# Kernel optimization log

Hardware: AMD Instinct MI355X
Metric: run time of the kernel (lower is better)

## Reference

```python
import jax, jax.numpy as jnp
import numpy as np

N_FILE, N_CLASS, N_FUNC = 50_000, 150_000, 300_000
E = 300_000
D = 128
L = 2  # num_layers

# (src_type, dst_type, conv_idx, edge_arg_name); conv_idx: 0=file,1=file_call,2=own,3=call
RELATIONS = [
    ("FILE", "CLASS", 0, "e_f_own_c"),
    ("FILE", "FUNCTION", 0, "e_f_own_fn"),
    ("FILE", "FUNCTION", 1, "e_f_call_fn"),
    ("FILE", "FILE", 1, "e_f_imp_f"),
    ("FILE", "CLASS", 1, "e_f_imp_c"),
    ("FILE", "FUNCTION", 1, "e_f_imp_fn"),
    ("CLASS", "CLASS", 2, "e_c_own_c"),
    ("CLASS", "FUNCTION", 2, "e_c_own_fn"),
    ("FUNCTION", "CLASS", 2, "e_fn_own_c"),
    ("FUNCTION", "FUNCTION", 2, "e_fn_own_fn"),
    ("CLASS", "FUNCTION", 3, "e_c_call_fn"),
    ("CLASS", "CLASS", 3, "e_c_inh_c"),
    ("FUNCTION", "FUNCTION", 3, "e_fn_call_fn"),
]
N_OF = {"FILE": N_FILE, "CLASS": N_CLASS, "FUNCTION": N_FUNC}


def _edges(key, n_src, n_dst):
    k1, k2 = jax.random.split(key)
    src = jax.random.randint(k1, (E,), 0, n_src, dtype=jnp.int32)
    dst = jax.random.randint(k2, (E,), 0, n_dst, dtype=jnp.int32)
    return jnp.stack([src, dst])  # [2, E]


def setup_inputs() -> dict:
    key = jax.random.key(0)
    ks = jax.random.split(key, 20)
    inp = {
        "x_file": jax.random.normal(ks[0], (N_FILE, D), jnp.float32),
        "x_class": jax.random.normal(ks[1], (N_CLASS, D), jnp.float32),
        "x_func": jax.random.normal(ks[2], (N_FUNC, D), jnp.float32),
        "Wl": jax.random.normal(ks[3], (L, 4, D, D), jnp.float32) * 0.05,
        "bl": jax.random.normal(ks[4], (L, 4, D), jnp.float32) * 0.05,
        "Wr": jax.random.normal(ks[5], (L, 4, D, D), jnp.float32) * 0.05,
    }
    for i, (s, t, _ci, name) in enumerate(RELATIONS):
        inp[name] = _edges(ks[6 + i], N_OF[s], N_OF[t])
    return inp


def _sage(x_src, x_dst, edges, Wl_, bl_, Wr_):
    """SAGEConv with mean aggregation: lin_l(scatter_mean(x_src[src] -> dst)) + lin_r(x_dst)."""
    src, dst = edges[0], edges[1]
    n_dst = x_dst.shape[0]
    msg = x_src[src]  # [E, D] gather
    agg = jax.ops.segment_sum(msg, dst, num_segments=n_dst)  # [n_dst, D]
    cnt = jax.ops.segment_sum(jnp.ones((msg.shape[0],), msg.dtype), dst, num_segments=n_dst)
    mean = agg / jnp.maximum(cnt, 1.0)[:, None]  # degree-0 nodes -> 0
    return mean @ Wl_ + bl_ + x_dst @ Wr_


def _forward(x_file, x_class, x_func, Wl, bl, Wr, edge_dict):
    h = {"FILE": x_file, "CLASS": x_class, "FUNCTION": x_func}
    for layer in range(L):
        outs = {"FILE": [], "CLASS": [], "FUNCTION": []}
        for s, t, ci, name in RELATIONS:
            outs[t].append(
                _sage(h[s], h[t], edge_dict[name], Wl[layer, ci], bl[layer, ci], Wr[layer, ci])
            )
        # HeteroConv aggr='mean' across relations per dst type, then ReLU
        h = {t: jax.nn.relu(sum(v) / float(len(v))) for t, v in outs.items()}
    # original returns a dict; concatenate in fixed order FILE, CLASS, FUNCTION
    return jnp.concatenate([h["FILE"], h["CLASS"], h["FUNCTION"]], axis=0)


def reference(x_file, x_class, x_func, Wl, bl, Wr,
              e_f_own_c, e_f_own_fn, e_f_call_fn, e_f_imp_f, e_f_imp_c, e_f_imp_fn,
              e_c_own_c, e_c_own_fn, e_fn_own_c, e_fn_own_fn,
              e_c_call_fn, e_c_inh_c, e_fn_call_fn):
    edge_dict = {
        "e_f_own_c": e_f_own_c, "e_f_own_fn": e_f_own_fn, "e_f_call_fn": e_f_call_fn,
        "e_f_imp_f": e_f_imp_f, "e_f_imp_c": e_f_imp_c, "e_f_imp_fn": e_f_imp_fn,
        "e_c_own_c": e_c_own_c, "e_c_own_fn": e_c_own_fn, "e_fn_own_c": e_fn_own_c,
        "e_fn_own_fn": e_fn_own_fn, "e_c_call_fn": e_c_call_fn, "e_c_inh_c": e_c_inh_c,
        "e_fn_call_fn": e_fn_call_fn,
    }
    return _forward(x_file, x_class, x_func, Wl, bl, Wr, edge_dict)
```

## Files before the change

### kernel.cpp

```cpp
#include <hip/hip_runtime.h>
#include <hip/hip_bf16.h>
#include <stdint.h>

typedef unsigned short u16;
typedef unsigned int u32;

#define NFILE 50000
#define NCLASS 150000
#define NFUNC 300000
#define NTOT 500000
#define EDG 300000
#define NRELS 13
#define RTOT 2900000

typedef __attribute__((ext_vector_type(8))) short bf16x8;
typedef __attribute__((ext_vector_type(4))) float f32x4;

__device__ __forceinline__ u16 f2b(float v){
    u32 u = __float_as_uint(v);
    u += 0x7fffu + ((u >> 16) & 1u);
    return (u16)(u >> 16);
}
__device__ __forceinline__ float b2f(u16 b){
    return __uint_as_float(((u32)b) << 16);
}
__device__ __forceinline__ u32 pack2(float a, float b){
    return (u32)f2b(a) | ((u32)f2b(b) << 16);
}

struct EdgePtrs { const int* e[NRELS]; };
struct RelMeta  { int base[NRELS]; };

__global__ void prep_weights(const float* __restrict__ Wl, const float* __restrict__ bl,
                             const float* __restrict__ Wr,
                             u16* __restrict__ WlT, u16* __restrict__ WrSumT,
                             float* __restrict__ blSum){
    int tid = blockIdx.x * 256 + threadIdx.x;
    if (tid >= 2 * 16384) return;
    int l   = tid >> 14;
    int rem = tid & 16383;
    int n   = rem >> 7;
    int k   = rem & 127;
    const int m[3][4] = {{0,1,0,0},{1,1,2,1},{1,2,2,2}};
    #pragma unroll
    for (int ci = 0; ci < 4; ++ci){
        float w = Wl[(((l*4)+ci)*128 + k)*128 + n];
        WlT[((l*4+ci)*128 + n)*128 + k] = f2b(w);
    }
    #pragma unroll
    for (int t = 0; t < 3; ++t){
        float s = 0.f;
        #pragma unroll
        for (int ci = 0; ci < 4; ++ci)
            s += (float)m[t][ci] * Wr[(((l*4)+ci)*128 + k)*128 + n];
        WrSumT[((l*3+t)*128 + n)*128 + k] = f2b(s);
    }
    if (k == 0){
        #pragma unroll
        for (int t = 0; t < 3; ++t){
            float s = 0.f;
            #pragma unroll
            for (int ci = 0; ci < 4; ++ci)
                s += (float)m[t][ci] * bl[(l*4+ci)*128 + n];
            blSum[(l*3+t)*128 + n] = s;
        }
    }
}

__global__ void count_kernel(EdgePtrs ep, RelMeta rm, int* __restrict__ off){
    int rel = blockIdx.y;
    int e = blockIdx.x * 256 + threadIdx.x;
    if (e >= EDG) return;
    int dst = ep.e[rel][EDG + e];
    atomicAdd(&off[rm.base[rel] + dst], 1);
}

__global__ void scan1(int* __restrict__ data, int* __restrict__ bsums, int n){
    __shared__ int sd[256];
    int tid = threadIdx.x;
    long base = (long)blockIdx.x * 2048 + (long)tid * 8;
    int v[8]; int tot = 0;
    #pragma unroll
    for (int i = 0; i < 8; ++i){
        long ix = base + i;
        v[i] = (ix < n) ? data[ix] : 0;
        tot += v[i];
    }
    sd[tid] = tot;
    __syncthreads();
    for (int s = 1; s < 256; s <<= 1){
        int t = (tid >= s) ? sd[tid - s] : 0;
        __syncthreads();
        sd[tid] += t;
        __syncthreads();
    }
    int incl = sd[tid];
    int excl = incl - tot;
    if (tid == 255 && bsums) bsums[blockIdx.x] = incl;
    int run = excl;
    #pragma unroll
    for (int i = 0; i < 8; ++i){
        long ix = base + i;
        if (ix < n) data[ix] = run;
        run += v[i];
    }
}

__global__ void scan_add(int* __restrict__ data, const int* __restrict__ bsums, int n){
    long i = (long)blockIdx.x * 256 + threadIdx.x;
    if (i < n) data[i] += bsums[i >> 11];
}

__global__ void fill_kernel(EdgePtrs ep, RelMeta rm, int* __restrict__ off, int* __restrict__ csr){
    int rel = blockIdx.y;
    int e = blockIdx.x * 256 + threadIdx.x;
    if (e >= EDG) return;
    int src = ep.e[rel][e];
    int dst = ep.e[rel][EDG + e];
    int pos = atomicAdd(&off[rm.base[rel] + dst], 1);
    csr[pos] = src;
}

struct FusedArgs {
    const void* sp0[4];
    const void* sp1[4];
    int b0[4], b1[4], nR[4];
    const u16* wl[4];
    int nG;
    const u16* wself;
    const float* bias;
};

template<bool SRC32, bool FINAL>
__global__ __launch_bounds__(256) void fused_kernel(
    const int* __restrict__ off, const int* __restrict__ csr,
    FusedArgs fa, const void* __restrict__ xdst,
    void* __restrict__ outp, int nRows, float invR)
{
    __shared__ u16 wlds[16384];
    __shared__ u16 meanB[8192];
    int tid = threadIdx.x, wave = tid >> 6, lane = tid & 63;
    int row0 = blockIdx.x * 64;
    int rlo = lane & 15, blk = lane >> 4;

    f32x4 acc[8];
    #pragma unroll
    for (int nt = 0; nt < 8; ++nt) acc[nt] = (f32x4){0.f, 0.f, 0.f, 0.f};

    for (int g = 0; g < fa.nG; ++g){
        __syncthreads();
        {
            const u16* WT = fa.wl[g];
            #pragma unroll
            for (int c = 0; c < 8; ++c){
                int i = c * 2048 + tid * 8;
                int n = i >> 7;
                int boff = (i * 2) ^ ((n & 7) << 4);
                *(uint4*)((char*)wlds + boff) = *(const uint4*)((const char*)WT + (long)i * 2);
            }
        }
        for (int rr = 0; rr < 4; ++rr){
            int row = wave * 16 + rr * 4 + blk;
            long grow = (long)row0 + row;
            bool valid = grow < nRows;
            float a[8];
            #pragma unroll
            for (int k = 0; k < 8; ++k) a[k] = 0.f;
            for (int r = 0; r < fa.nR[g]; ++r){
                const void* sp = r ? fa.sp1[g] : fa.sp0[g];
                long gr = (long)(r ? fa.b1[g] : fa.b0[g]) + grow;
                int st = 0, en = 0;
                if (valid){ st = (gr > 0) ? off[gr - 1] : 0; en = off[gr]; }
                float s[8], s2[8];
                #pragma unroll
                for (int k = 0; k < 8; ++k){ s[k] = 0.f; s2[k] = 0.f; }
                int j = st;
                for (; j + 1 < en; j += 2){
                    long i0 = csr[j], i1 = csr[j + 1];
                    if (SRC32){
                        const float* p0 = (const float*)sp + i0 * 128 + rlo * 8;
                        const float* p1 = (const float*)sp + i1 * 128 + rlo * 8;
                        float4 u0 = *(const float4*)p0, u1 = *(const float4*)(p0 + 4);
                        float4 v0 = *(const float4*)p1, v1 = *(const float4*)(p1 + 4);
                        s[0] += u0.x; s[1] += u0.y; s[2] += u0.z; s[3] += u0.w;
                        s[4] += u1.x; s[5] += u1.y; s[6] += u1.z; s[7] += u1.w;
                        s2[0] += v0.x; s2[1] += v0.y; s2[2] += v0.z; s2[3] += v0.w;
                        s2[4] += v1.x; s2[5] += v1.y; s2[6] += v1.z; s2[7] += v1.w;
                    } else {
                        uint4 u = *(const uint4*)((const u16*)sp + i0 * 128 + rlo * 8);
                        uint4 v = *(const uint4*)((const u16*)sp + i1 * 128 + rlo * 8);
                        s[0] += b2f((u16)(u.x & 0xffff)); s[1] += b2f((u16)(u.x >> 16));
                        s[2] += b2f((u16)(u.y & 0xffff)); s[3] += b2f((u16)(u.y >> 16));
                        s[4] += b2f((u16)(u.z & 0xffff)); s[5] += b2f((u16)(u.z >> 16));
                        s[6] += b2f((u16)(u.w & 0xffff)); s[7] += b2f((u16)(u.w >> 16));
                        s2[0] += b2f((u16)(v.x & 0xffff)); s2[1] += b2f((u16)(v.x >> 16));
                        s2[2] += b2f((u16)(v.y & 0xffff)); s2[3] += b2f((u16)(v.y >> 16));
                        s2[4] += b2f((u16)(v.z & 0xffff)); s2[5] += b2f((u16)(v.z >> 16));
                        s2[6] += b2f((u16)(v.w & 0xffff)); s2[7] += b2f((u16)(v.w >> 16));
                    }
                }
                if (j < en){
                    long i0 = csr[j];
                    if (SRC32){
                        const float* p0 = (const float*)sp + i0 * 128 + rlo * 8;
                        float4 u0 = *(const float4*)p0, u1 = *(const float4*)(p0 + 4);
                        s[0] += u0.x; s[1] += u0.y; s[2] += u0.z; s[3] += u0.w;
                        s[4] += u1.x; s[5] += u1.y; s[6] += u1.z; s[7] += u1.w;
                    } else {
                        uint4 u = *(const uint4*)((const u16*)sp + i0 * 128 + rlo * 8);
                        s[0] += b2f((u16)(u.x & 0xffff)); s[1] += b2f((u16)(u.x >> 16));
                        s[2] += b2f((u16)(u.y & 0xffff)); s[3] += b2f((u16)(u.y >> 16));
                        s[4] += b2f((u16)(u.z & 0xffff)); s[5] += b2f((u16)(u.z >> 16));
                        s[6] += b2f((u16)(u.w & 0xffff)); s[7] += b2f((u16)(u.w >> 16));
                    }
                }
                if (en > st){
                    float inv = 1.f / (float)(en - st);
                    #pragma unroll
                    for (int k = 0; k < 8; ++k) a[k] += (s[k] + s2[k]) * inv;
                }
            }
            uint4 w;
            w.x = pack2(a[0], a[1]); w.y = pack2(a[2], a[3]);
            w.z = pack2(a[4], a[5]); w.w = pack2(a[6], a[7]);
            int boff = (row * 256 + rlo * 16) ^ ((row & 7) << 4);
            *(uint4*)((char*)meanB + boff) = w;
        }
        __syncthreads();
        int arow = wave * 16 + rlo;
        #pragma unroll
        for (int s4 = 0; s4 < 4; ++s4){
            int aoff = (arow * 256 + s4 * 64 + blk * 16) ^ ((arow & 7) << 4);
            bf16x8 afr = *(const bf16x8*)((const char*)meanB + aoff);
            #pragma unroll
            for (int nt = 0; nt < 8; ++nt){
                int n = nt * 16 + rlo;
                int boff = (n * 256 + s4 * 64 + blk * 16) ^ ((n & 7) << 4);
                bf16x8 bfr = *(const bf16x8*)((const char*)wlds + boff);
                acc[nt] = __builtin_amdgcn_mfma_f32_16x16x32_bf16(afr, bfr, acc[nt], 0, 0, 0);
            }
        }
    }

    __syncthreads();
    {
        const u16* WT = fa.wself;
        #pragma unroll
        for (int c = 0; c < 8; ++c){
            int i = c * 2048 + tid * 8;
            int n = i >> 7;
            int boff = (i * 2) ^ ((n & 7) << 4);
            *(uint4*)((char*)wlds + boff) = *(const uint4*)((const char*)WT + (long)i * 2);
        }
    }
    __syncthreads();
    {
        long arow = (long)row0 + wave * 16 + rlo;
        if (arow >= nRows) arow = nRows - 1;
        bf16x8 af[4];
        if (SRC32){
            const float* A = (const float*)xdst + arow * 128;
            #pragma unroll
            for (int s4 = 0; s4 < 4; ++s4){
                float4 u0 = *(const float4*)(A + s4 * 32 + blk * 8);
                float4 u1 = *(const float4*)(A + s4 * 32 + blk * 8 + 4);
                bf16x8 t;
                t[0] = (short)f2b(u0.x); t[1] = (short)f2b(u0.y);
                t[2] = (short)f2b(u0.z); t[3] = (short)f2b(u0.w);
                t[4] = (short)f2b(u1.x); t[5] = (short)f2b(u1.y);
                t[6] = (short)f2b(u1.z); t[7] = (short)f2b(u1.w);
                af[s4] = t;
            }
        } else {
            const u16* A = (const u16*)xdst + arow * 128;
            #pragma unroll
            for (int s4 = 0; s4 < 4; ++s4)
                af[s4] = *(const bf16x8*)(A + s4 * 32 + blk * 8);
        }
        #pragma unroll
        for (int s4 = 0; s4 < 4; ++s4){
            #pragma unroll
            for (int nt = 0; nt < 8; ++nt){
                int n = nt * 16 + rlo;
                int boff = (n * 256 + s4 * 64 + blk * 16) ^ ((n & 7) << 4);
                bf16x8 bfr = *(const bf16x8*)((const char*)wlds + boff);
                acc[nt] = __builtin_amdgcn_mfma_f32_16x16x32_bf16(af[s4], bfr, acc[nt], 0, 0, 0);
            }
        }
    }

    long rb = (long)row0 + wave * 16 + blk * 4;
    #pragma unroll
    for (int nt = 0; nt < 8; ++nt){
        int cx = nt * 16 + rlo;
        float b = fa.bias[cx];
        #pragma unroll
        for (int j = 0; j < 4; ++j){
            long r = rb + j;
            if (r < nRows){
                float v = fmaxf(0.f, (acc[nt][j] + b) * invR);
                if (FINAL) ((float*)outp)[r * 128 + cx] = v;
                else       ((u16*)outp)[r * 128 + cx] = f2b(v);
            }
        }
    }
}

extern "C" void kernel_launch(void* const* d_in, const int* in_sizes, int n_in,
                              void* d_out, int out_size, void* d_ws, size_t ws_size,
                              hipStream_t stream){
    const float* xF  = (const float*)d_in[0];
    const float* xC  = (const float*)d_in[1];
    const float* xFn = (const float*)d_in[2];
    const float* Wl  = (const float*)d_in[3];
    const float* bl  = (const float*)d_in[4];
    const float* Wr  = (const float*)d_in[5];

    static const int relDstT[NRELS] = {1,2,2,0,1,2,1,2,1,2,2,1,2};
    static const int relSrcT[NRELS] = {0,0,0,0,0,0,1,1,2,2,1,1,2};
    const int nOf[3] = {NFILE, NCLASS, NFUNC};

    EdgePtrs ep;
    for (int r = 0; r < NRELS; ++r) ep.e[r] = (const int*)d_in[6 + r];
    RelMeta rm;
    {
        int a = 0;
        for (int r = 0; r < NRELS; ++r){ rm.base[r] = a; a += nOf[relDstT[r]]; }
    }

    char* ws = (char*)d_ws;
    size_t wo = 0;
    auto walloc = [&](size_t bytes) -> void* {
        void* p = ws + wo;
        wo = (wo + bytes + 255) & ~(size_t)255;
        return p;
    };
    int* off    = (int*)walloc((size_t)RTOT * 4);
    int* bsums  = (int*)walloc(8192);
    int* csr    = (int*)walloc((size_t)NRELS * EDG * 4);
    u16* h1     = (u16*)walloc((size_t)NTOT * 128 * 2);
    u16* WlT    = (u16*)walloc(2 * 4 * 16384 * 2);
    u16* WrSumT = (u16*)walloc(2 * 3 * 16384 * 2);
    float* blSum= (float*)walloc(2 * 3 * 128 * 4);

    prep_weights<<<128, 256, 0, stream>>>(Wl, bl, Wr, WlT, WrSumT, blSum);

    hipMemsetAsync(off, 0, (size_t)RTOT * 4, stream);
    dim3 egrid((EDG + 255) / 256, NRELS);
    count_kernel<<<egrid, 256, 0, stream>>>(ep, rm, off);
    int nb1 = (RTOT + 2047) / 2048;
    scan1<<<nb1, 256, 0, stream>>>(off, bsums, RTOT);
    scan1<<<1, 256, 0, stream>>>(bsums, (int*)nullptr, nb1);
    scan_add<<<(RTOT + 255) / 256, 256, 0, stream>>>(off, bsums, RTOT);
    fill_kernel<<<egrid, 256, 0, stream>>>(ep, rm, off, csr);

    float* outSeg[3] = {
        (float*)d_out,
        (float*)d_out + (long)NFILE * 128,
        (float*)d_out + (long)(NFILE + NCLASS) * 128
    };
    u16* hSeg[3] = {
        h1,
        h1 + (long)NFILE * 128,
        h1 + (long)(NFILE + NCLASS) * 128
    };
    const void* xSeg[3] = {xF, xC, xFn};
    const float invR[3] = {1.f, 0.2f, 1.f / 7.f};

    struct GDef { int ci, r0, r1; };
    static const GDef gF [1] = {{1, 3, -1}};
    static const GDef gC [4] = {{0, 0, -1}, {1, 4, -1}, {2, 6, 8}, {3, 11, -1}};
    static const GDef gFn[4] = {{0, 1, -1}, {1, 2, 5}, {2, 7, 9}, {3, 10, 12}};
    const GDef* gdefs[3] = {gF, gC, gFn};
    const int nGof[3] = {1, 4, 4};

    for (int layer = 0; layer < 2; ++layer){
        bool l0 = (layer == 0);
        for (int t = 0; t < 3; ++t){
            FusedArgs fa;
            fa.nG = nGof[t];
            for (int g = 0; g < fa.nG; ++g){
                const GDef gd = gdefs[t][g];
                fa.wl[g] = WlT + (layer * 4 + gd.ci) * 16384;
                fa.b0[g] = rm.base[gd.r0];
                fa.sp0[g] = l0 ? xSeg[relSrcT[gd.r0]] : (const void*)hSeg[relSrcT[gd.r0]];
                if (gd.r1 >= 0){
                    fa.nR[g] = 2;
                    fa.b1[g] = rm.base[gd.r1];
                    fa.sp1[g] = l0 ? xSeg[relSrcT[gd.r1]] : (const void*)hSeg[relSrcT[gd.r1]];
                } else {
                    fa.nR[g] = 1;
                    fa.b1[g] = 0;
                    fa.sp1[g] = nullptr;
                }
            }
            for (int g = fa.nG; g < 4; ++g){
                fa.wl[g] = nullptr; fa.b0[g] = fa.b1[g] = fa.nR[g] = 0;
                fa.sp0[g] = fa.sp1[g] = nullptr;
            }
            fa.wself = WrSumT + (layer * 3 + t) * 16384;
            fa.bias  = blSum + (layer * 3 + t) * 128;

            int n = nOf[t];
            int gb = (n + 63) / 64;
            const void* xdst = l0 ? xSeg[t] : (const void*)hSeg[t];
            void* outp = l0 ? (void*)hSeg[t] : (void*)outSeg[t];
            if (l0) fused_kernel<true , false><<<gb, 256, 0, stream>>>(off, csr, fa, xdst, outp, n, invR[t]);
            else    fused_kernel<false, true ><<<gb, 256, 0, stream>>>(off, csr, fa, xdst, outp, n, invR[t]);
        }
    }
}
```

Measured before the change: 2.909 ms.

## Specialize fused SAGE kernel per node type and pair relation groups per phase

Replaces the runtime-looped fused kernel with one specialized per destination type, whose slot-to-group mapping is fixed at compile time. Mean aggregation for two groups now runs per phase into double shared buffers, and the first two neighbour gathers are issued unconditionally with clamped indices and zero weights to hide latency. Weight tiles are no longer staged in LDS; MFMA B fragments are read directly from global memory (cached). This cuts LDS usage and barriers to target higher occupancy (launch bounds 4). The cost is redundant gathers for low-degree nodes and uncoalesced global weight reads.

```diff
diff --git a/kernel.cpp b/kernel.cpp
--- a/kernel.cpp
+++ b/kernel.cpp
@@ -12,6 +12,7 @@
 #define EDG 300000
 #define NRELS 13
 #define RTOT 2900000
+#define CSRMAX (NRELS * EDG)
 
 typedef __attribute__((ext_vector_type(8))) short bf16x8;
 typedef __attribute__((ext_vector_type(4))) float f32x4;
@@ -121,24 +122,93 @@
     csr[pos] = src;
 }
 
-struct FusedArgs {
-    const void* sp0[4];
-    const void* sp1[4];
-    int b0[4], b1[4], nR[4];
-    const u16* wl[4];
-    int nG;
+
+template<int T> struct Meta;
+template<> struct Meta<0>{ static constexpr int NG=1, NS=1;
+    static constexpr int sg[1]={0}; };
+template<> struct Meta<1>{ static constexpr int NG=4, NS=5;
+    static constexpr int sg[5]={0,1,2,2,3}; };
+template<> struct Meta<2>{ static constexpr int NG=4, NS=7;
+    static constexpr int sg[7]={0,1,1,2,2,3,3}; };
+
+struct FA2 {
+    const void* sp[7];
+    int ob[7];
+    int ns[7];
+    const u16* wg[4];
     const u16* wself;
     const float* bias;
 };
 
-template<bool SRC32, bool FINAL>
-__global__ __launch_bounds__(256) void fused_kernel(
+template<bool SRC32>
+__device__ __forceinline__ void gadd(const void* sp, long idx, int rlo, float w, float a[8]){
+    if (SRC32){
+        const float* pp = (const float*)sp + idx * 128 + rlo * 8;
+        float4 u0 = *(const float4*)pp, u1 = *(const float4*)(pp + 4);
+        a[0] += w * u0.x; a[1] += w * u0.y; a[2] += w * u0.z; a[3] += w * u0.w;
+        a[4] += w * u1.x; a[5] += w * u1.y; a[6] += w * u1.z; a[7] += w * u1.w;
+    } else {
+        uint4 u = *(const uint4*)((const u16*)sp + idx * 128 + rlo * 8);
+        a[0] += w * b2f((u16)(u.x & 0xffff)); a[1] += w * b2f((u16)(u.x >> 16));
+        a[2] += w * b2f((u16)(u.y & 0xffff)); a[3] += w * b2f((u16)(u.y >> 16));
+        a[4] += w * b2f((u16)(u.z & 0xffff)); a[5] += w * b2f((u16)(u.z >> 16));
+        a[6] += w * b2f((u16)(u.w & 0xffff)); a[7] += w * b2f((u16)(u.w >> 16));
+    }
+}
+
+template<bool SRC32>
+__device__ __forceinline__ void slotAcc(const int* __restrict__ off, const int* __restrict__ csr,
+                                        const void* sp, int ob, int ns,
+                                        int grow, bool valid, int rlo, float a[8]){
+    int st = 0, en = 0;
+    if (valid){
+        long gr = (long)ob + grow;
+        st = (gr > 0) ? off[gr - 1] : 0;
+        en = off[gr];
+    }
+    int deg = en - st;
+    float sc = (deg > 0) ? 1.f / (float)deg : 0.f;
+    int p0 = min(st, CSRMAX - 1);
+    int i0 = csr[p0];
+    int i1 = csr[min(p0 + 1, CSRMAX - 1)];
+    i0 = min(i0, ns - 1);
+    i1 = min(i1, ns - 1);
+    float w0 = (deg >= 1) ? sc : 0.f;
+    float w1 = (deg >= 2) ? sc : 0.f;
+    gadd<SRC32>(sp, i0, rlo, w0, a);
+    gadd<SRC32>(sp, i1, rlo, w1, a);
+    #pragma unroll 1
+    for (int j = st + 2; j < en; ++j){
+        int ix = csr[j];
+        gadd<SRC32>(sp, ix, rlo, sc, a);
+    }
+}
+
+__device__ __forceinline__ void mfmaGrp(const u16* mbuf, const u16* __restrict__ W,
+                                        f32x4 acc[8], int wave, int rlo, int blk){
+    int arow = wave * 16 + rlo;
+    #pragma unroll
+    for (int s4 = 0; s4 < 4; ++s4){
+        int aoff = (arow * 256 + s4 * 64 + blk * 16) ^ ((arow & 7) << 4);
+        bf16x8 afr = *(const bf16x8*)((const char*)mbuf + aoff);
+        #pragma unroll
+        for (int nt = 0; nt < 8; ++nt){
+            int n = nt * 16 + rlo;
+            bf16x8 bfr = *(const bf16x8*)(W + n * 128 + s4 * 32 + blk * 8);
+            acc[nt] = __builtin_amdgcn_mfma_f32_16x16x32_bf16(afr, bfr, acc[nt], 0, 0, 0);
+        }
+    }
+}
+
+template<int T, bool SRC32, bool FINAL>
+__global__ __launch_bounds__(256, 4) void fused2(
     const int* __restrict__ off, const int* __restrict__ csr,
-    FusedArgs fa, const void* __restrict__ xdst,
-    void* __restrict__ outp, int nRows, float invR)
+    FA2 fa, const void* __restrict__ xdst, void* __restrict__ outp,
+    int nRows, float invR)
 {
-    __shared__ u16 wlds[16384];
-    __shared__ u16 meanB[8192];
+    using M = Meta<T>;
+    constexpr int NPH = (M::NG + 1) / 2;
+    __shared__ u16 mb[2][8192];
     int tid = threadIdx.x, wave = tid >> 6, lane = tid & 63;
     int row0 = blockIdx.x * 64;
     int rlo = lane & 15, blk = lane >> 4;
@@ -147,113 +217,51 @@
     #pragma unroll
     for (int nt = 0; nt < 8; ++nt) acc[nt] = (f32x4){0.f, 0.f, 0.f, 0.f};
 
-    for (int g = 0; g < fa.nG; ++g){
+    #pragma unroll
+    for (int p = 0; p < NPH; ++p){
+        bool hasB = (2 * p + 1) < M::NG;
         __syncthreads();
-        {
-            const u16* WT = fa.wl[g];
-            #pragma unroll
-            for (int c = 0; c < 8; ++c){
-                int i = c * 2048 + tid * 8;
-                int n = i >> 7;
-                int boff = (i * 2) ^ ((n & 7) << 4);
-                *(uint4*)((char*)wlds + boff) = *(const uint4*)((const char*)WT + (long)i * 2);
-            }
-        }
+        #pragma unroll 1
         for (int rr = 0; rr < 4; ++rr){
             int row = wave * 16 + rr * 4 + blk;
-            long grow = (long)row0 + row;
+            int grow = row0 + row;
             bool valid = grow < nRows;
-            float a[8];
-            #pragma unroll
-            for (int k = 0; k < 8; ++k) a[k] = 0.f;
-            for (int r = 0; r < fa.nR[g]; ++r){
-                const void* sp = r ? fa.sp1[g] : fa.sp0[g];
-                long gr = (long)(r ? fa.b1[g] : fa.b0[g]) + grow;
-                int st = 0, en = 0;
-                if (valid){ st = (gr > 0) ? off[gr - 1] : 0; en = off[gr]; }
-                float s[8], s2[8];
+            float aA[8];
+            #pragma unroll
+            for (int k = 0; k < 8; ++k) aA[k] = 0.f;
+            #pragma unroll
+            for (int s = 0; s < M::NS; ++s){
+                if (M::sg[s] != 2 * p) continue;
+                slotAcc<SRC32>(off, csr, fa.sp[s], fa.ob[s], fa.ns[s], grow, valid, rlo, aA);
+            }
+            {
+                uint4 w;
+                w.x = pack2(aA[0], aA[1]); w.y = pack2(aA[2], aA[3]);
+                w.z = pack2(aA[4], aA[5]); w.w = pack2(aA[6], aA[7]);
+                int boff = (row * 256 + rlo * 16) ^ ((row & 7) << 4);
+                *(uint4*)((char*)mb[0] + boff) = w;
+            }
+            if (hasB){
+                float aB[8];
                 #pragma unroll
-                for (int k = 0; k < 8; ++k){ s[k] = 0.f; s2[k] = 0.f; }
-                int j = st;
-                for (; j + 1 < en; j += 2){
-                    long i0 = csr[j], i1 = csr[j + 1];
-                    if (SRC32){
-                        const float* p0 = (const float*)sp + i0 * 128 + rlo * 8;
-                        const float* p1 = (const float*)sp + i1 * 128 + rlo * 8;
-                        float4 u0 = *(const float4*)p0, u1 = *(const float4*)(p0 + 4);
-                        float4 v0 = *(const float4*)p1, v1 = *(const float4*)(p1 + 4);
-                        s[0] += u0.x; s[1] += u0.y; s[2] += u0.z; s[3] += u0.w;
-                        s[4] += u1.x; s[5] += u1.y; s[6] += u1.z; s[7] += u1.w;
-                        s2[0] += v0.x; s2[1] += v0.y; s2[2] += v0.z; s2[3] += v0.w;
-                        s2[4] += v1.x; s2[5] += v1.y; s2[6] += v1.z; s2[7] += v1.w;
-                    } else {
-                        uint4 u = *(const uint4*)((const u16*)sp + i0 * 128 + rlo * 8);
-                        uint4 v = *(const uint4*)((const u16*)sp + i1 * 128 + rlo * 8);
-                        s[0] += b2f((u16)(u.x & 0xffff)); s[1] += b2f((u16)(u.x >> 16));
-                        s[2] += b2f((u16)(u.y & 0xffff)); s[3] += b2f((u16)(u.y >> 16));
-                        s[4] += b2f((u16)(u.z & 0xffff)); s[5] += b2f((u16)(u.z >> 16));
-                        s[6] += b2f((u16)(u.w & 0xffff)); s[7] += b2f((u16)(u.w >> 16));
-                        s2[0] += b2f((u16)(v.x & 0xffff)); s2[1] += b2f((u16)(v.x >> 16));
-                        s2[2] += b2f((u16)(v.y & 0xffff)); s2[3] += b2f((u16)(v.y >> 16));
-                        s2[4] += b2f((u16)(v.z & 0xffff)); s2[5] += b2f((u16)(v.z >> 16));
-                        s2[6] += b2f((u16)(v.w & 0xffff)); s2[7] += b2f((u16)(v.w >> 16));
-                    }
+                for (int k = 0; k < 8; ++k) aB[k] = 0.f;
+                #pragma unroll
+                for (int s = 0; s < M::NS; ++s){
+                    if (M::sg[s] != 2 * p + 1) continue;
+                    slotAcc<SRC32>(off, csr, fa.sp[s], fa.ob[s], fa.ns[s], grow, valid, rlo, aB);
                 }
-                if (j < en){
-                    long i0 = csr[j];
-                    if (SRC32){
-                        const float* p0 = (const float*)sp + i0 * 128 + rlo * 8;
-                        float4 u0 = *(const float4*)p0, u1 = *(const float4*)(p0 + 4);
-                        s[0] += u0.x; s[1] += u0.y; s[2] += u0.z; s[3] += u0.w;
-                        s[4] += u1.x; s[5] += u1.y; s[6] += u1.z; s[7] += u1.w;
-                    } else {
-                        uint4 u = *(const uint4*)((const u16*)sp + i0 * 128 + rlo * 8);
-                        s[0] += b2f((u16)(u.x & 0xffff)); s[1] += b2f((u16)(u.x >> 16));
-                        s[2] += b2f((u16)(u.y & 0xffff)); s[3] += b2f((u16)(u.y >> 16));
-                        s[4] += b2f((u16)(u.z & 0xffff)); s[5] += b2f((u16)(u.z >> 16));
-                        s[6] += b2f((u16)(u.w & 0xffff)); s[7] += b2f((u16)(u.w >> 16));
-                    }
-                }
-                if (en > st){
-                    float inv = 1.f / (float)(en - st);
-                    #pragma unroll
-                    for (int k = 0; k < 8; ++k) a[k] += (s[k] + s2[k]) * inv;
-                }
-            }
-            uint4 w;
-            w.x = pack2(a[0], a[1]); w.y = pack2(a[2], a[3]);
-            w.z = pack2(a[4], a[5]); w.w = pack2(a[6], a[7]);
-            int boff = (row * 256 + rlo * 16) ^ ((row & 7) << 4);
-            *(uint4*)((char*)meanB + boff) = w;
+                uint4 w;
+                w.x = pack2(aB[0], aB[1]); w.y = pack2(aB[2], aB[3]);
+                w.z = pack2(aB[4], aB[5]); w.w = pack2(aB[6], aB[7]);
+                int boff = (row * 256 + rlo * 16) ^ ((row & 7) << 4);
+                *(uint4*)((char*)mb[1] + boff) = w;
+            }
         }
         __syncthreads();
-        int arow = wave * 16 + rlo;
-        #pragma unroll
-        for (int s4 = 0; s4 < 4; ++s4){
-            int aoff = (arow * 256 + s4 * 64 + blk * 16) ^ ((arow & 7) << 4);
-            bf16x8 afr = *(const bf16x8*)((const char*)meanB + aoff);
-            #pragma unroll
-            for (int nt = 0; nt < 8; ++nt){
-                int n = nt * 16 + rlo;
-                int boff = (n * 256 + s4 * 64 + blk * 16) ^ ((n & 7) << 4);
-                bf16x8 bfr = *(const bf16x8*)((const char*)wlds + boff);
-                acc[nt] = __builtin_amdgcn_mfma_f32_16x16x32_bf16(afr, bfr, acc[nt], 0, 0, 0);
-            }
-        }
-    }
-
-    __syncthreads();
-    {
-        const u16* WT = fa.wself;
-        #pragma unroll
-        for (int c = 0; c < 8; ++c){
-            int i = c * 2048 + tid * 8;
-            int n = i >> 7;
-            int boff = (i * 2) ^ ((n & 7) << 4);
-            *(uint4*)((char*)wlds + boff) = *(const uint4*)((const char*)WT + (long)i * 2);
-        }
-    }
-    __syncthreads();
+        mfmaGrp(mb[0], fa.wg[2 * p], acc, wave, rlo, blk);
+        if (hasB) mfmaGrp(mb[1], fa.wg[2 * p + 1], acc, wave, rlo, blk);
+    }
+
     {
         long arow = (long)row0 + wave * 16 + rlo;
         if (arow >= nRows) arow = nRows - 1;
@@ -282,8 +290,7 @@
             #pragma unroll
             for (int nt = 0; nt < 8; ++nt){
                 int n = nt * 16 + rlo;
-                int boff = (n * 256 + s4 * 64 + blk * 16) ^ ((n & 7) << 4);
-                bf16x8 bfr = *(const bf16x8*)((const char*)wlds + boff);
+                bf16x8 bfr = *(const bf16x8*)(fa.wself + n * 128 + s4 * 32 + blk * 8);
                 acc[nt] = __builtin_amdgcn_mfma_f32_16x16x32_bf16(af[s4], bfr, acc[nt], 0, 0, 0);
             }
         }
@@ -367,37 +374,31 @@
     const void* xSeg[3] = {xF, xC, xFn};
     const float invR[3] = {1.f, 0.2f, 1.f / 7.f};
 
-    struct GDef { int ci, r0, r1; };
-    static const GDef gF [1] = {{1, 3, -1}};
-    static const GDef gC [4] = {{0, 0, -1}, {1, 4, -1}, {2, 6, 8}, {3, 11, -1}};
-    static const GDef gFn[4] = {{0, 1, -1}, {1, 2, 5}, {2, 7, 9}, {3, 10, 12}};
-    const GDef* gdefs[3] = {gF, gC, gFn};
+    static const int slotRelF [1] = {3};
+    static const int slotRelC [5] = {0, 4, 6, 8, 11};
+    static const int slotRelFn[7] = {1, 2, 5, 7, 9, 10, 12};
+    const int* slotRelOf[3] = {slotRelF, slotRelC, slotRelFn};
+    const int nSlotOf[3] = {1, 5, 7};
+    static const int ciF [1] = {1};
+    static const int ciC [4] = {0, 1, 2, 3};
+    static const int ciFn[4] = {0, 1, 2, 3};
+    const int* ciOf[3] = {ciF, ciC, ciFn};
     const int nGof[3] = {1, 4, 4};
 
     for (int layer = 0; layer < 2; ++layer){
         bool l0 = (layer == 0);
         for (int t = 0; t < 3; ++t){
-            FusedArgs fa;
-            fa.nG = nGof[t];
-            for (int g = 0; g < fa.nG; ++g){
-                const GDef gd = gdefs[t][g];
-                fa.wl[g] = WlT + (layer * 4 + gd.ci) * 16384;
-                fa.b0[g] = rm.base[gd.r0];
-                fa.sp0[g] = l0 ? xSeg[relSrcT[gd.r0]] : (const void*)hSeg[relSrcT[gd.r0]];
-                if (gd.r1 >= 0){
-                    fa.nR[g] = 2;
-                    fa.b1[g] = rm.base[gd.r1];
-                    fa.sp1[g] = l0 ? xSeg[relSrcT[gd.r1]] : (const void*)hSeg[relSrcT[gd.r1]];
-                } else {
-                    fa.nR[g] = 1;
-                    fa.b1[g] = 0;
-                    fa.sp1[g] = nullptr;
-                }
-            }
-            for (int g = fa.nG; g < 4; ++g){
-                fa.wl[g] = nullptr; fa.b0[g] = fa.b1[g] = fa.nR[g] = 0;
-                fa.sp0[g] = fa.sp1[g] = nullptr;
-            }
+            FA2 fa;
+            for (int s = 0; s < 7; ++s){ fa.sp[s] = nullptr; fa.ob[s] = 0; fa.ns[s] = 1; }
+            for (int s = 0; s < nSlotOf[t]; ++s){
+                int rel = slotRelOf[t][s];
+                int st_ = relSrcT[rel];
+                fa.sp[s] = l0 ? xSeg[st_] : (const void*)hSeg[st_];
+                fa.ob[s] = rm.base[rel];
+                fa.ns[s] = nOf[st_];
+            }
+            for (int g = 0; g < 4; ++g)
+                fa.wg[g] = (g < nGof[t]) ? (WlT + (layer * 4 + ciOf[t][g]) * 16384) : (const u16*)nullptr;
             fa.wself = WrSumT + (layer * 3 + t) * 16384;
             fa.bias  = blSum + (layer * 3 + t) * 128;
 
@@ -405,8 +406,19 @@
             int gb = (n + 63) / 64;
             const void* xdst = l0 ? xSeg[t] : (const void*)hSeg[t];
             void* outp = l0 ? (void*)hSeg[t] : (void*)outSeg[t];
-            if (l0) fused_kernel<true , false><<<gb, 256, 0, stream>>>(off, csr, fa, xdst, outp, n, invR[t]);
-            else    fused_kernel<false, true ><<<gb, 256, 0, stream>>>(off, csr, fa, xdst, outp, n, invR[t]);
-        }
-    }
-}
+            if (l0){
+                switch (t){
+                    case 0: fused2<0, true, false><<<gb, 256, 0, stream>>>(off, csr, fa, xdst, outp, n, invR[t]); break;
+                    case 1: fused2<1, true, false><<<gb, 256, 0, stream>>>(off, csr, fa, xdst, outp, n, invR[t]); break;
+                    case 2: fused2<2, true, false><<<gb, 256, 0, stream>>>(off, csr, fa, xdst, outp, n, invR[t]); break;
+                }
+            } else {
+                switch (t){
+                    case 0: fused2<0, false, true><<<gb, 256, 0, stream>>>(off, csr, fa, xdst, outp, n, invR[t]); break;
+                    case 1: fused2<1, false, true><<<gb, 256, 0, stream>>>(off, csr, fa, xdst, outp, n, invR[t]); break;
+                    case 2: fused2<2, false, true><<<gb, 256, 0, stream>>>(off, csr, fa, xdst, outp, n, invR[t]); break;
+                }
+            }
+        }
+    }
+}
```

Result: faster. 2.807 ms (-3.5%).
